# Kernel tuning notes

Measured on AMD Instinct MI355X. Metric: run time of the kernel, lower is better.

## Reference

```python
import jax, jax.numpy as jnp
import numpy as np

D_MODEL = 256
LATENT = 64
OBJ = 32
OUT_DIM = LATENT + OBJ  # 96
STEPS = 50
BETA_START = 1e-4
BETA_END = 0.02
LN_EPS = 1e-5


def _gru_layer(x, w_ih, w_hh, b_ih, b_hh):
    # x: [B, T, din]; weights in torch layout: [3*d, din], [3*d, d]
    B = x.shape[0]
    d = w_hh.shape[1]

    def step(h, xt):
        gi = xt @ w_ih.T + b_ih
        gh = h @ w_hh.T + b_hh
        i_r, i_z, i_n = jnp.split(gi, 3, axis=-1)
        h_r, h_z, h_n = jnp.split(gh, 3, axis=-1)
        r = jax.nn.sigmoid(i_r + h_r)
        z = jax.nn.sigmoid(i_z + h_z)
        n = jnp.tanh(i_n + r * h_n)
        h_new = (1.0 - z) * n + z * h
        return h_new, h_new

    h0 = jnp.zeros((B, d), x.dtype)
    _, ys = jax.lax.scan(step, h0, jnp.swapaxes(x, 0, 1))
    return jnp.swapaxes(ys, 0, 1)


def setup_inputs() -> dict:
    key = jax.random.key(0)
    ks = jax.random.split(key, 24)
    B, T = 8, 512
    D, IN = D_MODEL, OUT_DIM
    s = 0.02
    inp = {
        "z_seq": jax.random.normal(ks[0], (B, T, LATENT), jnp.float32),
        "o_seq": jax.random.normal(ks[1], (B, T, OBJ), jnp.float32),
        "in_proj_w": jax.random.normal(ks[2], (D, IN), jnp.float32) * s,
        "in_proj_b": jnp.zeros((D,), jnp.float32),
        "gru_wih0": jax.random.normal(ks[3], (3 * D, D), jnp.float32) * s,
        "gru_whh0": jax.random.normal(ks[4], (3 * D, D), jnp.float32) * s,
        "gru_bih0": jnp.zeros((3 * D,), jnp.float32),
        "gru_bhh0": jnp.zeros((3 * D,), jnp.float32),
        "gru_wih1": jax.random.normal(ks[5], (3 * D, D), jnp.float32) * s,
        "gru_whh1": jax.random.normal(ks[6], (3 * D, D), jnp.float32) * s,
        "gru_bih1": jnp.zeros((3 * D,), jnp.float32),
        "gru_bhh1": jnp.zeros((3 * D,), jnp.float32),
        "ln_g": jnp.ones((D,), jnp.float32),
        "ln_b": jnp.zeros((D,), jnp.float32),
        "time_w1": jax.random.normal(ks[7], (D, 1), jnp.float32) * s,
        "time_b1": jnp.zeros((D,), jnp.float32),
        "time_w2": jax.random.normal(ks[8], (D, D), jnp.float32) * s,
        "time_b2": jnp.zeros((D,), jnp.float32),
        "den_w1": jax.random.normal(ks[9], (2 * D, OUT_DIM + 2 * D), jnp.float32) * s,
        "den_b1": jnp.zeros((2 * D,), jnp.float32),
        "den_w2": jax.random.normal(ks[10], (2 * D, 2 * D), jnp.float32) * s,
        "den_b2": jnp.zeros((2 * D,), jnp.float32),
        "den_w3": jax.random.normal(ks[11], (OUT_DIM, 2 * D), jnp.float32) * s,
        "den_b3": jnp.zeros((OUT_DIM,), jnp.float32),
    }
    return inp


def _forward(z_seq, o_seq, in_proj_w, in_proj_b, gru_wih0, gru_whh0, gru_bih0,
             gru_bhh0, gru_wih1, gru_whh1, gru_bih1, gru_bhh1, ln_g, ln_b,
             time_w1, time_b1, time_w2, time_b2, den_w1, den_b1, den_w2,
             den_b2, den_w3, den_b3):
    # --- conditioning: concat -> in_proj -> 2-layer GRU -> LayerNorm
    x = jnp.concatenate([z_seq, o_seq], axis=-1)            # [B,T,in_dim]
    hcond = x @ in_proj_w.T + in_proj_b                     # [B,T,D]
    hcond = _gru_layer(hcond, gru_wih0, gru_whh0, gru_bih0, gru_bhh0)
    hcond = _gru_layer(hcond, gru_wih1, gru_whh1, gru_bih1, gru_bhh1)
    mu = jnp.mean(hcond, axis=-1, keepdims=True)
    var = jnp.mean(jnp.square(hcond - mu), axis=-1, keepdims=True)
    hcond = (hcond - mu) * jax.lax.rsqrt(var + LN_EPS) * ln_g + ln_b

    B, T, _ = hcond.shape

    # --- diffusion schedule buffers
    betas = jnp.linspace(BETA_START, BETA_END, STEPS, dtype=jnp.float32)
    alphas = 1.0 - betas
    alpha_bars = jnp.cumprod(alphas)
    sqrt_recip_alphas = jnp.sqrt(1.0 / alphas)

    noise_key = jax.random.key(42)
    x0 = jax.random.normal(jax.random.fold_in(noise_key, STEPS),
                           (B, T, OUT_DIM), jnp.float32)

    def body(x_t, step):
        # time embedding: t_norm is a scalar (same for every token), broadcast
        t_norm = step.astype(jnp.float32) / float(max(1, STEPS - 1))
        e = jax.nn.silu(t_norm * time_w1[:, 0] + time_b1)   # [D]
        t_emb = e @ time_w2.T + time_b2                     # [D]
        t_emb = jnp.broadcast_to(t_emb, (B, T, D_MODEL))

        inp = jnp.concatenate([x_t, hcond, t_emb], axis=-1)  # [B,T,96+2D]
        y = jax.nn.silu(inp @ den_w1.T + den_b1)
        y = jax.nn.silu(y @ den_w2.T + den_b2)
        eps_theta = y @ den_w3.T + den_b3                   # [B,T,96]

        beta_t = betas[step]
        coeff = beta_t / jnp.sqrt(1.0 - alpha_bars[step])
        mean = sqrt_recip_alphas[step] * (x_t - coeff * eps_theta)
        noise = jax.random.normal(jax.random.fold_in(noise_key, step),
                                  x_t.shape, x_t.dtype)
        x_next = jnp.where(step > 0, mean + jnp.sqrt(beta_t) * noise, mean)
        return x_next, None

    steps = jnp.arange(STEPS - 1, -1, -1)
    x_t, _ = jax.lax.scan(body, x0, steps)
    return x_t


def reference(z_seq, o_seq, in_proj_w, in_proj_b, gru_wih0, gru_whh0, gru_bih0,
              gru_bhh0, gru_wih1, gru_whh1, gru_bih1, gru_bhh1, ln_g, ln_b,
              time_w1, time_b1, time_w2, time_b2, den_w1, den_b1, den_w2,
              den_b2, den_w3, den_b3):
    x_t = _forward(z_seq, o_seq, in_proj_w, in_proj_b, gru_wih0, gru_whh0,
                   gru_bih0, gru_bhh0, gru_wih1, gru_whh1, gru_bih1, gru_bhh1,
                   ln_g, ln_b, time_w1, time_b1, time_w2, time_b2, den_w1,
                   den_b1, den_w2, den_b2, den_w3, den_b3)
    return x_t[..., :LATENT], x_t[..., LATENT:]
```

## Files before the change

### kernel.cpp

```cpp
#include <hip/hip_runtime.h>
#include <stdint.h>
#include <math.h>

#define DM    256
#define G3    768
#define TT    512
#define BB    8
#define MM    4096
#define OUTD  96
#define HH2   512
#define NSTEPS 50
#define NTOT  (MM*OUTD)
#define NZTOT ((NSTEPS+1)*NTOT)
#define CH    32
#define NCH   (TT/CH)

typedef _Float16 f16;
typedef _Float16 f16x2 __attribute__((ext_vector_type(2)));
typedef _Float16 f16x8 __attribute__((ext_vector_type(8)));
typedef float    f32x4 __attribute__((ext_vector_type(4)));

__device__ __forceinline__ void lds_barrier() {
  asm volatile("s_waitcnt lgkmcnt(0)" ::: "memory");
  __builtin_amdgcn_s_barrier();
}

__device__ __forceinline__ void wait_flag(const uint32_t* f, uint32_t target) {
  while (__hip_atomic_load(f, __ATOMIC_RELAXED, __HIP_MEMORY_SCOPE_AGENT) < target)
    __builtin_amdgcn_s_sleep(2);
  __builtin_amdgcn_fence(__ATOMIC_ACQUIRE, "agent");
}

__host__ __device__ inline void tf2x32(uint32_t k0, uint32_t k1,
                                       uint32_t x0, uint32_t x1,
                                       uint32_t& o0, uint32_t& o1)
{
  uint32_t ks2 = k0 ^ k1 ^ 0x1BD11BDAu;
#define ROTL(v,r) (((v)<<(r))|((v)>>(32-(r))))
#define RND(r) { x0 += x1; x1 = ROTL(x1,r); x1 ^= x0; }
  x0 += k0; x1 += k1;
  RND(13) RND(15) RND(26) RND(6)
  x0 += k1;  x1 += ks2 + 1u;
  RND(17) RND(29) RND(16) RND(24)
  x0 += ks2; x1 += k0 + 2u;
  RND(13) RND(15) RND(26) RND(6)
  x0 += k0;  x1 += k1 + 3u;
  RND(17) RND(29) RND(16) RND(24)
  x0 += k1;  x1 += ks2 + 4u;
  RND(13) RND(15) RND(26) RND(6)
  x0 += ks2; x1 += k0 + 5u;
  o0 = x0; o1 = x1;
#undef RND
#undef ROTL
}

__device__ inline float bits_to_normal(uint32_t bits) {
  float f = __uint_as_float((bits >> 9) | 0x3F800000u) - 1.0f;
  const float lo = -0.99999994f;
  float u = fmaxf(lo, f * 2.0f + lo);
  float w = -log1pf(-u * u);
  float p;
  if (w < 5.0f) {
    w -= 2.5f;
    p = 2.81022636e-08f;
    p = fmaf(p, w, 3.43273939e-07f);
    p = fmaf(p, w, -3.5233877e-06f);
    p = fmaf(p, w, -4.39150654e-06f);
    p = fmaf(p, w, 0.00021858087f);
    p = fmaf(p, w, -0.00125372503f);
    p = fmaf(p, w, -0.00417768164f);
    p = fmaf(p, w, 0.246640727f);
    p = fmaf(p, w, 1.50140941f);
  } else {
    w = sqrtf(w) - 3.0f;
    p = -0.000200214257f;
    p = fmaf(p, w, 0.000100950558f);
    p = fmaf(p, w, 0.00134934322f);
    p = fmaf(p, w, -0.00367342844f);
    p = fmaf(p, w, 0.00573950773f);
    p = fmaf(p, w, -0.0076224613f);
    p = fmaf(p, w, 0.00943887047f);
    p = fmaf(p, w, 1.00167406f);
    p = fmaf(p, w, 2.83297682f);
  }
  float ei = p * u;
  return 1.41421356f * ei;
}

__device__ inline float jax_normal_elem(uint32_t k0, uint32_t k1, uint32_t e) {
  uint32_t o0, o1;
  tf2x32(k0, k1, 0u, e, o0, o1);
  return bits_to_normal(o0 ^ o1);
}

__device__ inline float dot2f(f16x2 a, f16x2 b, float c) {
#if __has_builtin(__builtin_amdgcn_fdot2)
  return __builtin_amdgcn_fdot2(a, b, c, false);
#else
  return c + (float)a[0]*(float)b[0] + (float)a[1]*(float)b[1];
#endif
}
__device__ inline float sigmoidf_(float x) { return 1.f / (1.f + __expf(-x)); }
__device__ inline float siluf_(float x)    { return x / (1.f + __expf(-x)); }
__device__ inline float tanhf_(float x) {
  float e = __expf(-2.f * fabsf(x));
  float t = (1.f - e) / (1.f + e);
  return copysignf(t, x);
}

__device__ inline unsigned char f32_to_e4m3(float f) {
#if __has_builtin(__builtin_amdgcn_cvt_pk_fp8_f32)
  int p = __builtin_amdgcn_cvt_pk_fp8_f32(f, f, 0, false);
  return (unsigned char)(p & 0xff);
#else
  uint32_t u = __float_as_uint(f);
  unsigned char s = (unsigned char)((u >> 24) & 0x80);
  float af = fabsf(f);
  if (!(af == af)) return (unsigned char)(s | 0x7f);
  if (af >= 448.f) return (unsigned char)(s | 0x7e);
  if (af < 0.0078125f) {
    int q = (int)rintf(af * 512.f);
    return (unsigned char)(s | q);
  }
  int e; float m = frexpf(af, &e);
  int mant = (int)rintf(m * 16.f);
  if (mant == 16) { mant = 8; e += 1; }
  int E = e - 1 + 7;
  if (E <= 0) { int q = (int)rintf(af * 512.f); return (unsigned char)(s | q); }
  return (unsigned char)(s | (E << 3) | (mant - 8));
#endif
}

struct DiffParams {
  float sra[NSTEPS], coeff[NSTEPS], sb[NSTEPS];
  uint32_t k0[NSTEPS], k1[NSTEPS];
  uint32_t xk0, xk1;
};

template<bool WF, bool WH, bool PUB, bool WAIT>
__device__ __forceinline__ void scan_body(int b, int d,
    const float* __restrict__ gi, const f16* __restrict__ whh,
    const float* __restrict__ bhh,
    float* __restrict__ hf_out, f16* __restrict__ hh_out,
    f16 (*hbuf)[128], uint32_t* pubf, const uint32_t* waitf)
{
  f16x8 wr[16], wz[16], wn[16];
  {
    const f16x8* pr = (const f16x8*)(whh + (size_t)d*DM);
    const f16x8* pz = (const f16x8*)(whh + (size_t)(256+d)*DM);
    const f16x8* pn = (const f16x8*)(whh + (size_t)(512+d)*DM);
    #pragma unroll
    for (int q = 0; q < 16; q++) { wr[q]=pr[q]; wz[q]=pz[q]; wn[q]=pn[q]; }
  }
  if (d < 128) { hbuf[0][d] = (f16)0.f; hbuf[1][d] = (f16)0.f; }
  const float bn = bhh[512 + d];
  float h_old = 0.f;
  __syncthreads();
  const size_t rowbase = (size_t)b * TT;
  if (WAIT) wait_flag(waitf, 2u * 2u);
  float gr[4], gz[4], gn[4];
  #pragma unroll
  for (int i = 0; i < 3; i++) {
    const float* gp = gi + (rowbase + i)*G3;
    gr[i] = gp[d]; gz[i] = gp[256+d]; gn[i] = gp[512+d];
  }
  #pragma unroll 4
  for (int t = 0; t < TT; t++) {
    if (WAIT && t && (t & (CH-1)) == 0) {
      int c = t >> 5;
      int nc = c + 2 > NCH ? NCH : c + 2;
      wait_flag(waitf, 2u * (uint32_t)nc);
    }
    const int sl = t & 3;
    const int sl3 = (t + 3) & 3;
    if (t + 3 < TT) {
      const float* gp = gi + (rowbase + t + 3)*G3;
      gr[sl3] = gp[d]; gz[sl3] = gp[256+d]; gn[sl3] = gp[512+d];
    }
    float ar0=0.f, ar1=0.f, az0=0.f, az1=0.f, an0=0.f, an1=0.f;
    const f16x8* hb = (const f16x8*)hbuf[t & 1];
    #pragma unroll
    for (int q = 0; q < 16; q++) {
      f16x8 hv = hb[q];
      f16x8 w0 = wr[q], w1 = wz[q], w2 = wn[q];
      #pragma unroll
      for (int pp = 0; pp < 4; pp++) {
        f16x2 ha; ha[0]=hv[2*pp]; ha[1]=hv[2*pp+1];
        f16x2 vr; vr[0]=w0[2*pp]; vr[1]=w0[2*pp+1];
        f16x2 vz; vz[0]=w1[2*pp]; vz[1]=w1[2*pp+1];
        f16x2 vn; vn[0]=w2[2*pp]; vn[1]=w2[2*pp+1];
        if (pp & 1) { ar1=dot2f(ha,vr,ar1); az1=dot2f(ha,vz,az1); an1=dot2f(ha,vn,an1); }
        else        { ar0=dot2f(ha,vr,ar0); az0=dot2f(ha,vz,az0); an0=dot2f(ha,vn,an0); }
      }
    }
    float rr = sigmoidf_((ar0+ar1) + gr[sl]);
    float zz = sigmoidf_((az0+az1) + gz[sl]);
    float nv = tanhf_(gn[sl] + rr * ((an0+an1) + bn));
    float hn = (1.f - zz) * nv + zz * h_old;
    h_old = hn;
    if (d < 128) hbuf[(t & 1) ^ 1][d] = (f16)hn;
    size_t o = (rowbase + t)*DM + d;
    if (WF) hf_out[o] = hn;
    if (WH) hh_out[o] = (f16)hn;
    if (PUB && ((t + 1) & (CH-1)) == 0) {
      __syncthreads();
      if (d == 0)
        __hip_atomic_store(pubf, (uint32_t)(t + 1), __ATOMIC_RELEASE,
                           __HIP_MEMORY_SCOPE_AGENT);
    } else {
      lds_barrier();
    }
  }
}

__global__ __launch_bounds__(256)
void k_inproj_mega(const float* __restrict__ z, const float* __restrict__ o,
                   const float* __restrict__ W, const float* __restrict__ b,
                   f16* __restrict__ hh,
                   const float* __restrict__ wih0, f16* __restrict__ wih0h,
                   const float* __restrict__ whh0, f16* __restrict__ whh0h,
                   const float* __restrict__ bih0, const float* __restrict__ bhh0,
                   float* __restrict__ cb0,
                   const float* __restrict__ wih1, f16* __restrict__ wih1h,
                   const float* __restrict__ whh1, f16* __restrict__ whh1h,
                   const float* __restrict__ bih1, const float* __restrict__ bhh1,
                   float* __restrict__ cb1, uint32_t* __restrict__ flags)
{
  const int blk = blockIdx.x, d = threadIdx.x;
  __shared__ float xs[96];
  if (blk < MM) {
    const int m = blk;
    if (d < 64) xs[d] = z[m*64 + d];
    else if (d < 96) xs[d] = o[m*32 + d - 64];
    __syncthreads();
    const float* wr = W + d*96;
    float acc = b[d];
    #pragma unroll
    for (int k = 0; k < 96; k++) acc = fmaf(xs[k], wr[k], acc);
    hh[m*DM + d] = (f16)acc;
  } else if (blk < MM + 96) {
    for (int i = (blk - MM)*256 + d; i < G3*DM; i += 96*256) wih0h[i] = (f16)wih0[i];
  } else if (blk < MM + 192) {
    for (int i = (blk - MM - 96)*256 + d; i < G3*DM; i += 96*256) whh0h[i] = (f16)whh0[i];
  } else if (blk == MM + 192) {
    for (int j = d; j < G3; j += 256) cb0[j] = bih0[j] + (j < 512 ? bhh0[j] : 0.f);
  } else if (blk < MM + 289) {
    for (int i = (blk - MM - 193)*256 + d; i < G3*DM; i += 96*256) wih1h[i] = (f16)wih1[i];
  } else if (blk < MM + 385) {
    for (int i = (blk - MM - 289)*256 + d; i < G3*DM; i += 96*256) whh1h[i] = (f16)whh1[i];
  } else if (blk == MM + 385) {
    for (int j = d; j < G3; j += 256) cb1[j] = bih1[j] + (j < 512 ? bhh1[j] : 0.f);
  } else {
    if (d < 16) flags[d] = 0u;
  }
}

__global__ __launch_bounds__(256, 1)
void k_scan_pipe(const float* __restrict__ gi, float* __restrict__ gi1,
                 const f16* __restrict__ whh0h, const float* __restrict__ bhh0,
                 f16* __restrict__ h0h,
                 const f16* __restrict__ wih1h, const float* __restrict__ cb1,
                 const f16* __restrict__ whh1h, const float* __restrict__ bhh1,
                 float* __restrict__ hf_out,
                 uint32_t* __restrict__ flags,
                 const float* __restrict__ dw2, unsigned char* __restrict__ w2p,
                 const float* __restrict__ dw3, f16* __restrict__ w3h,
                 const float* __restrict__ dw1, f16* __restrict__ w1x,
                 f16* __restrict__ w1h,
                 const float* __restrict__ tw1, const float* __restrict__ tb1,
                 const float* __restrict__ tw2, const float* __restrict__ tb2,
                 const float* __restrict__ db1, float* __restrict__ tv,
                 f16* __restrict__ nzb, DiffParams P)
{
  __shared__ f16 hbuf[2][128];
  __shared__ float e[DM], te[DM];
  const int blk = blockIdx.x, t = threadIdx.x;
  if (blk < 8) {
    scan_body<false, true, true, false>(blk, t, gi, whh0h, bhh0,
                                        nullptr, h0h, hbuf, &flags[blk], nullptr);
  } else if (blk < 24) {
    const int g = blk - 8, b = g >> 1, nh = g & 1;
    const int lane = t & 63, wave = t >> 6;
    const int mt = wave & 1, ng = wave >> 1;
    const int n0w = nh*384 + ng*192;
    const int l15 = lane & 15, kq = (lane >> 4)*8;
    const int rb = (lane >> 4)*4;
    for (int c = 0; c < NCH; c++) {
      wait_flag(&flags[b], (uint32_t)((c + 1)*CH));
      const int mrow = c*CH + mt*16 + l15;
      const f16* Ap = h0h + ((size_t)b*TT + mrow)*DM + kq;
      f32x4 acc[12] = {};
      #pragma unroll
      for (int kt = 0; kt < 8; kt++) {
        f16x8 a = *(const f16x8*)(Ap + kt*32);
        #pragma unroll
        for (int nt = 0; nt < 12; nt++) {
          const f16* Bp = wih1h + (size_t)(n0w + nt*16 + l15)*DM + kq + kt*32;
          acc[nt] = __builtin_amdgcn_mfma_f32_16x16x32_f16(a, *(const f16x8*)Bp, acc[nt], 0,0,0);
        }
      }
      #pragma unroll
      for (int nt = 0; nt < 12; nt++) {
        int n = n0w + nt*16 + l15;
        float bb = cb1[n];
        #pragma unroll
        for (int r = 0; r < 4; r++) {
          int m = c*CH + mt*16 + rb + r;
          gi1[((size_t)b*TT + m)*G3 + n] = acc[nt][r] + bb;
        }
      }
      __syncthreads();
      if (t == 0)
        __hip_atomic_fetch_add(&flags[8 + b], 1u, __ATOMIC_RELEASE,
                               __HIP_MEMORY_SCOPE_AGENT);
    }
  } else if (blk < 32) {
    const int b = blk - 24;
    scan_body<true, false, false, true>(b, t, gi1, whh1h, bhh1,
                                        hf_out, nullptr, hbuf, nullptr, &flags[8 + b]);
  } else if (blk < 96) {
    for (int i = (blk - 32)*256 + t; i < 512*512; i += 64*256) {
      int j = i & 7;
      int lane = (i >> 3) & 63;
      int tk = i >> 9;
      int tt = tk >> 4, kt = tk & 15;
      int row = tt*16 + (lane & 15);
      int col = kt*32 + (lane >> 4)*8 + j;
      w2p[i] = f32_to_e4m3(dw2[row*512 + col]);
    }
  } else if (blk < 112) {
    for (int i = (blk - 96)*256 + t; i < OUTD*HH2; i += 16*256) w3h[i] = (f16)dw3[i];
  } else if (blk < 168) {
    for (int i = (blk - 112)*256 + t; i < 512*96 + 512*256; i += 56*256) {
      if (i < 512*96) { int n = i/96, k = i%96; w1x[i] = (f16)dw1[n*608 + k]; }
      else { int jj = i - 512*96; int n = jj/256, k = jj%256; w1h[jj] = (f16)dw1[n*608 + 96 + k]; }
    }
  } else if (blk < 218) {
    const int s = blk - 168;
    float tn = (float)s / 49.f;
    { float v = tn * tw1[t] + tb1[t]; e[t] = siluf_(v); }
    __syncthreads();
    {
      float acc = tb2[t];
      const float* wr = tw2 + t*DM;
      #pragma unroll 8
      for (int k = 0; k < DM; k++) acc = fmaf(e[k], wr[k], acc);
      te[t] = acc;
    }
    __syncthreads();
    for (int n = t; n < HH2; n += 256) {
      float a2 = db1[n];
      const float* r = dw1 + n*608 + 352;
      #pragma unroll 8
      for (int k = 0; k < DM; k++) a2 = fmaf(te[k], r[k], a2);
      tv[s*HH2 + n] = a2;
    }
  } else {
    long base = (long)(blk - 218) * 9792;
    long end  = base + 9792;
    while (base < end) {
      int s = (int)(base / NTOT);
      long segend = (long)(s + 1) * NTOT;
      if (segend > end) segend = end;
      uint32_t kk0 = (s < NSTEPS) ? P.k0[s] : P.xk0;
      uint32_t kk1 = (s < NSTEPS) ? P.k1[s] : P.xk1;
      long sbase = (long)s * NTOT;
      for (long ee = base + t; ee < segend; ee += 256)
        nzb[ee] = (f16)jax_normal_elem(kk0, kk1, (uint32_t)(ee - sbase));
      base = segend;
    }
  }
}

__global__ __launch_bounds__(256)
void k_ln(const float* __restrict__ h, const float* __restrict__ g,
          const float* __restrict__ bb, f16* __restrict__ out)
{
  int m = blockIdx.x, d = threadIdx.x;
  float v = h[m*DM + d];
  __shared__ float r1[4], r2[4];
  float s = v;
  #pragma unroll
  for (int o = 32; o; o >>= 1) s += __shfl_down(s, o, 64);
  if ((d & 63) == 0) r1[d >> 6] = s;
  __syncthreads();
  float mu = (r1[0]+r1[1]+r1[2]+r1[3]) * (1.f/256.f);
  float dv = v - mu;
  float q = dv * dv;
  #pragma unroll
  for (int o = 32; o; o >>= 1) q += __shfl_down(q, o, 64);
  if ((d & 63) == 0) r2[d >> 6] = q;
  __syncthreads();
  float var = (r2[0]+r2[1]+r2[2]+r2[3]) * (1.f/256.f);
  out[m*DM + d] = (f16)(dv * rsqrtf(var + 1e-5f) * g[d] + bb[d]);
}

constexpr int EPI_F32 = 0, EPI_F32_BIAS = 1, EPI_F16 = 4;

template<int NT, int EPI, int KTILES>
__global__ __launch_bounds__(256, 2)
void k_gemm(const f16* __restrict__ A, const f16* __restrict__ Bw,
            int K, int N,
            const float* __restrict__ bias,
            float* __restrict__ Yf, f16* __restrict__ Yh)
{
  const int lane = threadIdx.x & 63;
  const int wave = threadIdx.x >> 6;
  const int m0 = blockIdx.y * 64 + wave * 16;
  const int n0 = blockIdx.x * (16 * NT);
  const int mrow = m0 + (lane & 15);
  const int kq = (lane >> 4) * 8;
  f32x4 acc[NT] = {};
  const f16* Ap = A + (long)mrow * K + kq;
  #pragma unroll
  for (int kt = 0; kt < KTILES; kt++) {
    f16x8 a = *(const f16x8*)(Ap + kt*32);
    #pragma unroll
    for (int nt = 0; nt < NT; nt++) {
      const f16* Bp = Bw + (long)(n0 + nt*16 + (lane & 15)) * K + kq + kt*32;
      acc[nt] = __builtin_amdgcn_mfma_f32_16x16x32_f16(a, *(const f16x8*)Bp, acc[nt], 0, 0, 0);
    }
  }
  const int rb = (lane >> 4) * 4;
  #pragma unroll
  for (int nt = 0; nt < NT; nt++) {
    int n = n0 + nt*16 + (lane & 15);
    #pragma unroll
    for (int r = 0; r < 4; r++) {
      int m = m0 + rb + r;
      float v = acc[nt][r];
      if (EPI == EPI_F32)            { Yf[(long)m*N + n] = v; }
      else if (EPI == EPI_F32_BIAS)  { v += bias[n]; Yf[(long)m*N + n] = v; }
      else                           { Yh[(long)m*N + n] = (f16)v; }
    }
  }
}

#define YSTR  520
#define XHSTR 104
#define W3STR 520

__device__ __forceinline__ int y1p_swz(int g) {
  return ((g >> 2) & 7) | ((g & 3) << 3) | (g & 32);
}

__global__ __launch_bounds__(1024)
void k_diff(const f16* __restrict__ w1x,
            const unsigned char* __restrict__ w2p,
            const f16* __restrict__ w3h,
            const f16* __restrict__ hpreh,
            const float* __restrict__ tv,
            const float* __restrict__ db2,
            const float* __restrict__ db3,
            const f16* __restrict__ nzb,
            float* __restrict__ out,
            DiffParams P)
{
  __shared__ unsigned char y1p_l[16*512];
  __shared__ f16 y2_l[16*YSTR];
  __shared__ f16 xh_l[16*XHSTR];
  __shared__ f16 w3_l[96*W3STR];

  const int t = threadIdx.x;
  const int lane = t & 63;
  const int wave = t >> 6;
  const int quad = lane >> 4;
  const int l15 = lane & 15;
  const int m0 = blockIdx.x * 16;
  const int n0w = wave * 32;

  const int t0 = 2*wave, t1 = 2*wave + 1;
  const int lsw8 = y1p_swz(lane) << 3;

  long w2f0[16], w2f1[16];
  {
    const unsigned char* p0 = w2p + (((size_t)(t0*16)*64 + lane) << 3);
    const unsigned char* p1 = w2p + (((size_t)(t1*16)*64 + lane) << 3);
    #pragma unroll
    for (int kt = 0; kt < 16; kt++) {
      w2f0[kt] = *(const long*)(p0 + kt*512);
      w2f1[kt] = *(const long*)(p1 + kt*512);
    }
  }
  float hpr[2][4];
  #pragma unroll
  for (int nt = 0; nt < 2; nt++)
    #pragma unroll
    for (int r = 0; r < 4; r++)
      hpr[nt][r] = (float)hpreh[(long)(m0 + quad*4 + r)*HH2 + n0w + nt*16 + l15];
  const float db2r0 = db2[n0w + l15];
  const float db2r1 = db2[n0w + 16 + l15];

  #pragma unroll
  for (int i = 0; i < 6; i++) {
    int v = t + i*1024;
    int row = v >> 6, c8 = v & 63;
    *((f16x8*)&w3_l[row*W3STR] + c8) = *((const f16x8*)(w3h + row*HH2) + c8);
  }

  const int neps = wave * 16 + l15;
  float xreg[4];
  if (wave < 6) {
    #pragma unroll
    for (int r = 0; r < 4; r++) {
      int ml = quad*4 + r;
      float v = (float)nzb[(size_t)NSTEPS*NTOT + (size_t)(m0 + ml)*OUTD + neps];
      xreg[r] = v;
      xh_l[ml*XHSTR + neps] = (f16)v;
    }
  }

  for (int s = NSTEPS-1; s >= 0; --s) {
    __syncthreads();
    f16 nzr[4];
    if (wave < 6 && s > 0) {
      #pragma unroll
      for (int r = 0; r < 4; r++)
        nzr[r] = nzb[(size_t)s*NTOT + (size_t)(m0 + quad*4 + r)*OUTD + neps];
    }
    {
      f32x4 acc[2] = {};
      #pragma unroll
      for (int kt = 0; kt < 3; kt++) {
        f16x8 a = *(const f16x8*)&xh_l[l15*XHSTR + kt*32 + quad*8];
        f16x8 b0 = *(const f16x8*)&w1x[(n0w + l15)*96 + kt*32 + quad*8];
        f16x8 b1 = *(const f16x8*)&w1x[(n0w + 16 + l15)*96 + kt*32 + quad*8];
        acc[0] = __builtin_amdgcn_mfma_f32_16x16x32_f16(a, b0, acc[0], 0,0,0);
        acc[1] = __builtin_amdgcn_mfma_f32_16x16x32_f16(a, b1, acc[1], 0,0,0);
      }
      #pragma unroll
      for (int nt = 0; nt < 2; nt++) {
        int n = n0w + nt*16 + l15;
        float tvv = tv[s*HH2 + n];
        int lp = ((nt*2 + (l15>>3)) << 4);
        int jp = l15 & 7;
        #pragma unroll
        for (int r = 0; r < 4; r++) {
          float v = (nt ? acc[1][r] : acc[0][r]) + hpr[nt][r] + tvv;
          int ml = quad*4 + r;
          y1p_l[wave*512 + (y1p_swz(ml | lp) << 3) + jp] = f32_to_e4m3(siluf_(v));
        }
      }
    }
    lds_barrier();
    {
      f32x4 acc2[2] = {};
      #pragma unroll
      for (int kt = 0; kt < 16; kt++) {
        long a  = *(const long*)(y1p_l + kt*512 + lsw8);
        acc2[0] = __builtin_amdgcn_mfma_f32_16x16x32_fp8_fp8(a, w2f0[kt], acc2[0], 0,0,0);
        acc2[1] = __builtin_amdgcn_mfma_f32_16x16x32_fp8_fp8(a, w2f1[kt], acc2[1], 0,0,0);
      }
      #pragma unroll
      for (int nt = 0; nt < 2; nt++) {
        int n = n0w + nt*16 + l15;
        float bb = nt ? db2r1 : db2r0;
        #pragma unroll
        for (int r = 0; r < 4; r++) {
          int ml = quad*4 + r;
          y2_l[ml*YSTR + n] = (f16)siluf_((nt ? acc2[1][r] : acc2[0][r]) + bb);
        }
      }
    }
    lds_barrier();
    if (wave < 6) {
      f32x4 acc3 = {};
      #pragma unroll 8
      for (int kt = 0; kt < 16; kt++) {
        f16x8 a = *(const f16x8*)&y2_l[l15*YSTR + kt*32 + quad*8];
        f16x8 b = *(const f16x8*)&w3_l[(wave*16 + l15)*W3STR + kt*32 + quad*8];
        acc3 = __builtin_amdgcn_mfma_f32_16x16x32_f16(a, b, acc3, 0,0,0);
      }
      float sra = P.sra[s], coeff = P.coeff[s], sb = P.sb[s];
      float b3 = db3[neps];
      #pragma unroll
      for (int r = 0; r < 4; r++) {
        int ml = quad*4 + r;
        float eps = acc3[r] + b3;
        float mean = sra * (xreg[r] - coeff * eps);
        float xn = mean;
        if (s > 0) xn = mean + sb * (float)nzr[r];
        xreg[r] = xn;
        xh_l[ml*XHSTR + neps] = (f16)xn;
      }
    }
  }
  if (wave < 6) {
    #pragma unroll
    for (int r = 0; r < 4; r++) {
      long m = m0 + quad*4 + r;
      if (neps < 64) out[m*64 + neps] = xreg[r];
      else out[(long)MM*64 + m*32 + (neps - 64)] = xreg[r];
    }
  }
}

extern "C" void kernel_launch(void* const* d_in, const int* in_sizes, int n_in,
                              void* d_out, int out_size, void* d_ws, size_t ws_size,
                              hipStream_t stream)
{
  (void)in_sizes; (void)n_in; (void)out_size; (void)ws_size;
  const float* z_seq = (const float*)d_in[0];
  const float* o_seq = (const float*)d_in[1];
  const float* in_w  = (const float*)d_in[2];
  const float* in_b  = (const float*)d_in[3];
  const float* wih0  = (const float*)d_in[4];
  const float* whh0  = (const float*)d_in[5];
  const float* bih0  = (const float*)d_in[6];
  const float* bhh0  = (const float*)d_in[7];
  const float* wih1  = (const float*)d_in[8];
  const float* whh1  = (const float*)d_in[9];
  const float* bih1  = (const float*)d_in[10];
  const float* bhh1  = (const float*)d_in[11];
  const float* ln_g  = (const float*)d_in[12];
  const float* ln_b  = (const float*)d_in[13];
  const float* tw1   = (const float*)d_in[14];
  const float* tb1   = (const float*)d_in[15];
  const float* tw2   = (const float*)d_in[16];
  const float* tb2   = (const float*)d_in[17];
  const float* dw1   = (const float*)d_in[18];
  const float* db1   = (const float*)d_in[19];
  const float* dw2   = (const float*)d_in[20];
  const float* db2   = (const float*)d_in[21];
  const float* dw3   = (const float*)d_in[22];
  const float* db3   = (const float*)d_in[23];

  char* base = (char*)d_ws;
  size_t off = 0;
  auto alloc = [&](size_t bytes) -> void* {
    void* p = base + off;
    off = (off + bytes + 255) & ~(size_t)255;
    return p;
  };
  float* gi     = (float*)alloc((size_t)MM*G3*4);
  float* hA     = (float*)alloc((size_t)MM*DM*4);
  f16*   hAh    = (f16*)  alloc((size_t)MM*DM*2);
  f16*   hpreh  = (f16*)  alloc((size_t)MM*HH2*2);
  f16*   hcondh = (f16*)  alloc((size_t)MM*DM*2);
  float* tv     = (float*)alloc((size_t)NSTEPS*HH2*4);
  f16*   wih0h  = (f16*)  alloc((size_t)G3*DM*2);
  f16*   whh0h  = (f16*)  alloc((size_t)G3*DM*2);
  f16*   wih1h  = (f16*)  alloc((size_t)G3*DM*2);
  f16*   whh1h  = (f16*)  alloc((size_t)G3*DM*2);
  f16*   w1xh   = (f16*)  alloc((size_t)HH2*96*2);
  f16*   w1hh   = (f16*)  alloc((size_t)HH2*DM*2);
  unsigned char* w2p = (unsigned char*)alloc((size_t)HH2*HH2);
  f16*   w3h    = (f16*)  alloc((size_t)OUTD*HH2*2);
  float* cb0    = (float*)alloc((size_t)G3*4);
  float* cb1    = (float*)alloc((size_t)G3*4);
  uint32_t* flags = (uint32_t*)alloc(64);
  f16*   nzb    = (f16*)  alloc((size_t)NZTOT*2);

  DiffParams P;
  {
    float ab = 1.f;
    float delta = (0.02f - 1e-4f) / 49.f;
    for (int i = 0; i < NSTEPS; i++) {
      float bt = 1e-4f + delta * (float)i;
      float al = 1.f - bt;
      ab *= al;
      P.sra[i]   = sqrtf(1.f / al);
      P.coeff[i] = bt / sqrtf(1.f - ab);
      P.sb[i]    = sqrtf(bt);
    }
    for (int s = 0; s < NSTEPS; s++) {
      uint32_t o0, o1;
      tf2x32(0u, 42u, 0u, (uint32_t)s, o0, o1);
      P.k0[s] = o0; P.k1[s] = o1;
    }
    uint32_t o0, o1;
    tf2x32(0u, 42u, 0u, (uint32_t)NSTEPS, o0, o1);
    P.xk0 = o0; P.xk1 = o1;
  }

  k_inproj_mega<<<MM + 387, 256, 0, stream>>>(
      z_seq, o_seq, in_w, in_b, hAh,
      wih0, wih0h, whh0, whh0h, bih0, bhh0, cb0,
      wih1, wih1h, whh1, whh1h, bih1, bhh1, cb1, flags);
  k_gemm<4, EPI_F32_BIAS, 8><<<dim3(12, 64), 256, 0, stream>>>(
      hAh, wih0h, DM, G3, cb0, gi, nullptr);
  k_scan_pipe<<<218 + 2048, 256, 0, stream>>>(
      gi, gi, whh0h, bhh0, hAh,
      wih1h, cb1, whh1h, bhh1, hA, flags,
      dw2, w2p, dw3, w3h, dw1, w1xh, w1hh,
      tw1, tb1, tw2, tb2, db1, tv, nzb, P);
  k_ln<<<MM, 256, 0, stream>>>(hA, ln_g, ln_b, hcondh);
  k_gemm<4, EPI_F16, 8><<<dim3(8, 64), 256, 0, stream>>>(
      hcondh, w1hh, DM, HH2, nullptr, nullptr, hpreh);
  k_diff<<<256, 1024, 0, stream>>>(w1xh, w2p, w3h, hpreh, tv, db2, db3, nzb,
                                   (float*)d_out, P);
}
```

Baseline: 848.4 us.

## Fold input GEMM and LayerNorm+W1h GEMM into the pipelined persistent scan kernel

The standalone layer-0 input-gate GEMM now runs as chunked producer blocks inside the persistent scan kernel, with flags so the layer-0 scan starts as soon as the first chunk is ready. The separate LayerNorm and hidden-projection GEMM kernels become per-chunk consumer blocks that wait on the layer-1 scan flags, so that work overlaps the recurrence. The chunk size is halved to shorten pipeline fill, and both layers' gate buffers share one array. This removes three launches and their serialization, at the cost of more spin-wait flag traffic and a dependence on all spinning blocks being co-resident.

```diff
diff --git a/kernel.cpp b/kernel.cpp
--- a/kernel.cpp
+++ b/kernel.cpp
@@ -12,8 +12,13 @@
 #define NSTEPS 50
 #define NTOT  (MM*OUTD)
 #define NZTOT ((NSTEPS+1)*NTOT)
-#define CH    32
+#define CH    16
 #define NCH   (TT/CH)
+#define F0 0
+#define F1 8
+#define F2 16
+#define F3 24
+#define FW1 32
 
 typedef _Float16 f16;
 typedef _Float16 f16x2 __attribute__((ext_vector_type(2)));
@@ -167,7 +172,7 @@
   #pragma unroll 4
   for (int t = 0; t < TT; t++) {
     if (WAIT && t && (t & (CH-1)) == 0) {
-      int c = t >> 5;
+      int c = t / CH;
       int nc = c + 2 > NCH ? NCH : c + 2;
       wait_flag(waitf, 2u * (uint32_t)nc);
     }
@@ -210,6 +215,42 @@
     } else {
       lds_barrier();
     }
+  }
+}
+
+__device__ __forceinline__ void gi_gemm_chunks(int b, int nh, int t,
+    const f16* __restrict__ A, const f16* __restrict__ Bw,
+    const float* __restrict__ bias, float* __restrict__ Y,
+    const uint32_t* waitf, uint32_t* pubf)
+{
+  const int lane = t & 63, wave = t >> 6;
+  const int n0w = nh*384 + wave*96;
+  const int l15 = lane & 15, quad = lane >> 4;
+  const int kq = quad*8, rb = quad*4;
+  for (int c = 0; c < NCH; c++) {
+    if (waitf) wait_flag(waitf, (uint32_t)((c+1)*CH));
+    const f16* Ap = A + ((size_t)b*TT + c*CH + l15)*DM + kq;
+    f32x4 acc[6] = {};
+    #pragma unroll
+    for (int kt = 0; kt < 8; kt++) {
+      f16x8 a = *(const f16x8*)(Ap + kt*32);
+      #pragma unroll
+      for (int nt = 0; nt < 6; nt++) {
+        const f16* Bp = Bw + (size_t)(n0w + nt*16 + l15)*DM + kq + kt*32;
+        acc[nt] = __builtin_amdgcn_mfma_f32_16x16x32_f16(a, *(const f16x8*)Bp, acc[nt], 0,0,0);
+      }
+    }
+    #pragma unroll
+    for (int nt = 0; nt < 6; nt++) {
+      int n = n0w + nt*16 + l15;
+      float bb = bias[n];
+      #pragma unroll
+      for (int r = 0; r < 4; r++)
+        Y[((size_t)b*TT + c*CH + rb + r)*G3 + n] = acc[nt][r] + bb;
+    }
+    __syncthreads();
+    if (t == 0)
+      __hip_atomic_fetch_add(pubf, 1u, __ATOMIC_RELEASE, __HIP_MEMORY_SCOPE_AGENT);
   }
 }
 
@@ -251,17 +292,20 @@
   } else if (blk == MM + 385) {
     for (int j = d; j < G3; j += 256) cb1[j] = bih1[j] + (j < 512 ? bhh1[j] : 0.f);
   } else {
-    if (d < 16) flags[d] = 0u;
+    if (d < 33) flags[d] = 0u;
   }
 }
 
 __global__ __launch_bounds__(256, 1)
-void k_scan_pipe(const float* __restrict__ gi, float* __restrict__ gi1,
+void k_scan_pipe(float* __restrict__ gi,
                  const f16* __restrict__ whh0h, const float* __restrict__ bhh0,
                  f16* __restrict__ h0h,
+                 const f16* __restrict__ wih0h, const float* __restrict__ cb0,
                  const f16* __restrict__ wih1h, const float* __restrict__ cb1,
                  const f16* __restrict__ whh1h, const float* __restrict__ bhh1,
-                 float* __restrict__ hf_out,
+                 float* __restrict__ hA,
+                 const float* __restrict__ ln_g, const float* __restrict__ ln_b,
+                 const f16* __restrict__ w1hh, f16* __restrict__ hpreh,
                  uint32_t* __restrict__ flags,
                  const float* __restrict__ dw2, unsigned char* __restrict__ w2p,
                  const float* __restrict__ dw3, f16* __restrict__ w3h,
@@ -274,52 +318,26 @@
 {
   __shared__ f16 hbuf[2][128];
   __shared__ float e[DM], te[DM];
+  __shared__ f16 hc[16][264];
   const int blk = blockIdx.x, t = threadIdx.x;
-  if (blk < 8) {
-    scan_body<false, true, true, false>(blk, t, gi, whh0h, bhh0,
-                                        nullptr, h0h, hbuf, &flags[blk], nullptr);
+  if (blk < 16) {
+    const int b = blk >> 1, nh = blk & 1;
+    gi_gemm_chunks(b, nh, t, h0h, wih0h, cb0, gi, nullptr, &flags[F3 + b]);
   } else if (blk < 24) {
-    const int g = blk - 8, b = g >> 1, nh = g & 1;
-    const int lane = t & 63, wave = t >> 6;
-    const int mt = wave & 1, ng = wave >> 1;
-    const int n0w = nh*384 + ng*192;
-    const int l15 = lane & 15, kq = (lane >> 4)*8;
-    const int rb = (lane >> 4)*4;
-    for (int c = 0; c < NCH; c++) {
-      wait_flag(&flags[b], (uint32_t)((c + 1)*CH));
-      const int mrow = c*CH + mt*16 + l15;
-      const f16* Ap = h0h + ((size_t)b*TT + mrow)*DM + kq;
-      f32x4 acc[12] = {};
-      #pragma unroll
-      for (int kt = 0; kt < 8; kt++) {
-        f16x8 a = *(const f16x8*)(Ap + kt*32);
-        #pragma unroll
-        for (int nt = 0; nt < 12; nt++) {
-          const f16* Bp = wih1h + (size_t)(n0w + nt*16 + l15)*DM + kq + kt*32;
-          acc[nt] = __builtin_amdgcn_mfma_f32_16x16x32_f16(a, *(const f16x8*)Bp, acc[nt], 0,0,0);
-        }
-      }
-      #pragma unroll
-      for (int nt = 0; nt < 12; nt++) {
-        int n = n0w + nt*16 + l15;
-        float bb = cb1[n];
-        #pragma unroll
-        for (int r = 0; r < 4; r++) {
-          int m = c*CH + mt*16 + rb + r;
-          gi1[((size_t)b*TT + m)*G3 + n] = acc[nt][r] + bb;
-        }
-      }
-      __syncthreads();
-      if (t == 0)
-        __hip_atomic_fetch_add(&flags[8 + b], 1u, __ATOMIC_RELEASE,
-                               __HIP_MEMORY_SCOPE_AGENT);
-    }
-  } else if (blk < 32) {
-    const int b = blk - 24;
-    scan_body<true, false, false, true>(b, t, gi1, whh1h, bhh1,
-                                        hf_out, nullptr, hbuf, nullptr, &flags[8 + b]);
-  } else if (blk < 96) {
-    for (int i = (blk - 32)*256 + t; i < 512*512; i += 64*256) {
+    const int b = blk - 16;
+    scan_body<false, true, true, true>(b, t, gi, whh0h, bhh0,
+                                       nullptr, h0h, hbuf,
+                                       &flags[F0 + b], &flags[F3 + b]);
+  } else if (blk < 40) {
+    const int g = blk - 24, b = g >> 1, nh = g & 1;
+    gi_gemm_chunks(b, nh, t, h0h, wih1h, cb1, gi, &flags[F0 + b], &flags[F1 + b]);
+  } else if (blk < 48) {
+    const int b = blk - 40;
+    scan_body<true, false, true, true>(b, t, gi, whh1h, bhh1,
+                                       hA, nullptr, hbuf,
+                                       &flags[F2 + b], &flags[F1 + b]);
+  } else if (blk < 112) {
+    for (int i = (blk - 48)*256 + t; i < 512*512; i += 64*256) {
       int j = i & 7;
       int lane = (i >> 3) & 63;
       int tk = i >> 9;
@@ -328,15 +346,18 @@
       int col = kt*32 + (lane >> 4)*8 + j;
       w2p[i] = f32_to_e4m3(dw2[row*512 + col]);
     }
-  } else if (blk < 112) {
-    for (int i = (blk - 96)*256 + t; i < OUTD*HH2; i += 16*256) w3h[i] = (f16)dw3[i];
-  } else if (blk < 168) {
-    for (int i = (blk - 112)*256 + t; i < 512*96 + 512*256; i += 56*256) {
+  } else if (blk < 128) {
+    for (int i = (blk - 112)*256 + t; i < OUTD*HH2; i += 16*256) w3h[i] = (f16)dw3[i];
+  } else if (blk < 184) {
+    for (int i = (blk - 128)*256 + t; i < 512*96 + 512*256; i += 56*256) {
       if (i < 512*96) { int n = i/96, k = i%96; w1x[i] = (f16)dw1[n*608 + k]; }
       else { int jj = i - 512*96; int n = jj/256, k = jj%256; w1h[jj] = (f16)dw1[n*608 + 96 + k]; }
     }
-  } else if (blk < 218) {
-    const int s = blk - 168;
+    __syncthreads();
+    if (t == 0)
+      __hip_atomic_fetch_add(&flags[FW1], 1u, __ATOMIC_RELEASE, __HIP_MEMORY_SCOPE_AGENT);
+  } else if (blk < 234) {
+    const int s = blk - 184;
     float tn = (float)s / 49.f;
     { float v = tn * tw1[t] + tb1[t]; e[t] = siluf_(v); }
     __syncthreads();
@@ -355,8 +376,55 @@
       for (int k = 0; k < DM; k++) a2 = fmaf(te[k], r[k], a2);
       tv[s*HH2 + n] = a2;
     }
+  } else if (blk < 490) {
+    const int g = blk - 234, b = g >> 5, c = g & 31;
+    wait_flag(&flags[FW1], 56u);
+    wait_flag(&flags[F2 + b], (uint32_t)((c+1)*CH));
+    const int wave = t >> 6, lane = t & 63;
+    const size_t R0 = (size_t)b*TT + c*CH;
+    float gl0=ln_g[lane], gl1=ln_g[lane+64], gl2=ln_g[lane+128], gl3=ln_g[lane+192];
+    float bl0=ln_b[lane], bl1=ln_b[lane+64], bl2=ln_b[lane+128], bl3=ln_b[lane+192];
+    #pragma unroll
+    for (int rr = 0; rr < 4; rr++) {
+      int r = wave*4 + rr;
+      const float* row = hA + (R0 + r)*DM;
+      float v0=row[lane], v1=row[lane+64], v2=row[lane+128], v3=row[lane+192];
+      float s = v0+v1+v2+v3;
+      #pragma unroll
+      for (int o2 = 32; o2; o2 >>= 1) s += __shfl_xor(s, o2, 64);
+      float mu = s * (1.f/256.f);
+      float d0=v0-mu, d1=v1-mu, d2=v2-mu, d3=v3-mu;
+      float q = d0*d0+d1*d1+d2*d2+d3*d3;
+      #pragma unroll
+      for (int o2 = 32; o2; o2 >>= 1) q += __shfl_xor(q, o2, 64);
+      float rs = rsqrtf(q*(1.f/256.f) + 1e-5f);
+      hc[r][lane]     = (f16)(d0*rs*gl0 + bl0);
+      hc[r][lane+64]  = (f16)(d1*rs*gl1 + bl1);
+      hc[r][lane+128] = (f16)(d2*rs*gl2 + bl2);
+      hc[r][lane+192] = (f16)(d3*rs*gl3 + bl3);
+    }
+    __syncthreads();
+    const int l15 = lane & 15, quad = lane >> 4;
+    const int kq = quad*8, rb = quad*4;
+    f32x4 acc[8] = {};
+    #pragma unroll
+    for (int kt = 0; kt < 8; kt++) {
+      f16x8 a = *(const f16x8*)&hc[l15][kt*32 + kq];
+      #pragma unroll
+      for (int nt = 0; nt < 8; nt++) {
+        const f16* Bp = w1hh + (size_t)(wave*128 + nt*16 + l15)*DM + kq + kt*32;
+        acc[nt] = __builtin_amdgcn_mfma_f32_16x16x32_f16(a, *(const f16x8*)Bp, acc[nt], 0,0,0);
+      }
+    }
+    #pragma unroll
+    for (int nt = 0; nt < 8; nt++) {
+      int n = wave*128 + nt*16 + l15;
+      #pragma unroll
+      for (int r = 0; r < 4; r++)
+        hpreh[(R0 + rb + r)*HH2 + n] = (f16)acc[nt][r];
+    }
   } else {
-    long base = (long)(blk - 218) * 9792;
+    long base = (long)(blk - 490) * 9792;
     long end  = base + 9792;
     while (base < end) {
       int s = (int)(base / NTOT);
@@ -368,70 +436,6 @@
       for (long ee = base + t; ee < segend; ee += 256)
         nzb[ee] = (f16)jax_normal_elem(kk0, kk1, (uint32_t)(ee - sbase));
       base = segend;
-    }
-  }
-}
-
-__global__ __launch_bounds__(256)
-void k_ln(const float* __restrict__ h, const float* __restrict__ g,
-          const float* __restrict__ bb, f16* __restrict__ out)
-{
-  int m = blockIdx.x, d = threadIdx.x;
-  float v = h[m*DM + d];
-  __shared__ float r1[4], r2[4];
-  float s = v;
-  #pragma unroll
-  for (int o = 32; o; o >>= 1) s += __shfl_down(s, o, 64);
-  if ((d & 63) == 0) r1[d >> 6] = s;
-  __syncthreads();
-  float mu = (r1[0]+r1[1]+r1[2]+r1[3]) * (1.f/256.f);
-  float dv = v - mu;
-  float q = dv * dv;
-  #pragma unroll
-  for (int o = 32; o; o >>= 1) q += __shfl_down(q, o, 64);
-  if ((d & 63) == 0) r2[d >> 6] = q;
-  __syncthreads();
-  float var = (r2[0]+r2[1]+r2[2]+r2[3]) * (1.f/256.f);
-  out[m*DM + d] = (f16)(dv * rsqrtf(var + 1e-5f) * g[d] + bb[d]);
-}
-
-constexpr int EPI_F32 = 0, EPI_F32_BIAS = 1, EPI_F16 = 4;
-
-template<int NT, int EPI, int KTILES>
-__global__ __launch_bounds__(256, 2)
-void k_gemm(const f16* __restrict__ A, const f16* __restrict__ Bw,
-            int K, int N,
-            const float* __restrict__ bias,
-            float* __restrict__ Yf, f16* __restrict__ Yh)
-{
-  const int lane = threadIdx.x & 63;
-  const int wave = threadIdx.x >> 6;
-  const int m0 = blockIdx.y * 64 + wave * 16;
-  const int n0 = blockIdx.x * (16 * NT);
-  const int mrow = m0 + (lane & 15);
-  const int kq = (lane >> 4) * 8;
-  f32x4 acc[NT] = {};
-  const f16* Ap = A + (long)mrow * K + kq;
-  #pragma unroll
-  for (int kt = 0; kt < KTILES; kt++) {
-    f16x8 a = *(const f16x8*)(Ap + kt*32);
-    #pragma unroll
-    for (int nt = 0; nt < NT; nt++) {
-      const f16* Bp = Bw + (long)(n0 + nt*16 + (lane & 15)) * K + kq + kt*32;
-      acc[nt] = __builtin_amdgcn_mfma_f32_16x16x32_f16(a, *(const f16x8*)Bp, acc[nt], 0, 0, 0);
-    }
-  }
-  const int rb = (lane >> 4) * 4;
-  #pragma unroll
-  for (int nt = 0; nt < NT; nt++) {
-    int n = n0 + nt*16 + (lane & 15);
-    #pragma unroll
-    for (int r = 0; r < 4; r++) {
-      int m = m0 + rb + r;
-      float v = acc[nt][r];
-      if (EPI == EPI_F32)            { Yf[(long)m*N + n] = v; }
-      else if (EPI == EPI_F32_BIAS)  { v += bias[n]; Yf[(long)m*N + n] = v; }
-      else                           { Yh[(long)m*N + n] = (f16)v; }
     }
   }
 }
@@ -636,7 +640,6 @@
   float* hA     = (float*)alloc((size_t)MM*DM*4);
   f16*   hAh    = (f16*)  alloc((size_t)MM*DM*2);
   f16*   hpreh  = (f16*)  alloc((size_t)MM*HH2*2);
-  f16*   hcondh = (f16*)  alloc((size_t)MM*DM*2);
   float* tv     = (float*)alloc((size_t)NSTEPS*HH2*4);
   f16*   wih0h  = (f16*)  alloc((size_t)G3*DM*2);
   f16*   whh0h  = (f16*)  alloc((size_t)G3*DM*2);
@@ -648,7 +651,7 @@
   f16*   w3h    = (f16*)  alloc((size_t)OUTD*HH2*2);
   float* cb0    = (float*)alloc((size_t)G3*4);
   float* cb1    = (float*)alloc((size_t)G3*4);
-  uint32_t* flags = (uint32_t*)alloc(64);
+  uint32_t* flags = (uint32_t*)alloc(256);
   f16*   nzb    = (f16*)  alloc((size_t)NZTOT*2);
 
   DiffParams P;
@@ -677,16 +680,12 @@
       z_seq, o_seq, in_w, in_b, hAh,
       wih0, wih0h, whh0, whh0h, bih0, bhh0, cb0,
       wih1, wih1h, whh1, whh1h, bih1, bhh1, cb1, flags);
-  k_gemm<4, EPI_F32_BIAS, 8><<<dim3(12, 64), 256, 0, stream>>>(
-      hAh, wih0h, DM, G3, cb0, gi, nullptr);
-  k_scan_pipe<<<218 + 2048, 256, 0, stream>>>(
-      gi, gi, whh0h, bhh0, hAh,
-      wih1h, cb1, whh1h, bhh1, hA, flags,
+  k_scan_pipe<<<490 + 2048, 256, 0, stream>>>(
+      gi, whh0h, bhh0, hAh, wih0h, cb0,
+      wih1h, cb1, whh1h, bhh1, hA,
+      ln_g, ln_b, w1hh, hpreh, flags,
       dw2, w2p, dw3, w3h, dw1, w1xh, w1hh,
       tw1, tb1, tw2, tb2, db1, tv, nzb, P);
-  k_ln<<<MM, 256, 0, stream>>>(hA, ln_g, ln_b, hcondh);
-  k_gemm<4, EPI_F16, 8><<<dim3(8, 64), 256, 0, stream>>>(
-      hcondh, w1hh, DM, HH2, nullptr, nullptr, hpreh);
   k_diff<<<256, 1024, 0, stream>>>(w1xh, w2p, w3h, hpreh, tv, db2, db3, nzb,
                                    (float*)d_out, P);
 }
```

Result: slower. 1.042 ms (+22.9%).
